# Kernel tuning notes

Measured on AMD Instinct MI355X. Metric: run time of the kernel, lower is better.

## Reference

```python
import jax, jax.numpy as jnp
import numpy as np
import math

H = 2048          # hidden_size
NH = 16           # num_attn_heads
HD = H // NH      # attn head dim = 128
NFW = 4           # num_lact_heads
FD = H // NFW     # fw head dim = 512
DH = FD           # inter_multi = 1.0
CHUNK = 512       # lact_chunk_size
WINDOW = 2048     # window_size
ROPE_BASE = 500000.0
BASE_LR_INV = math.log(math.expm1(0.001))  # inv_softplus(1e-3)


def rmsnorm(x, w, eps=1e-6):
    return x * jax.lax.rsqrt(jnp.mean(x * x, axis=-1, keepdims=True) + eps) * w


def l2norm(x, eps=1e-12):
    return x * jax.lax.rsqrt(jnp.sum(x * x, axis=-1, keepdims=True) + eps)


def rope(x):  # x: [b, h, s, d], half-split convention
    d = x.shape[-1]
    s = x.shape[2]
    inv = 1.0 / (ROPE_BASE ** (jnp.arange(d // 2, dtype=jnp.float32) / (d // 2)))
    f = jnp.arange(s, dtype=jnp.float32)[:, None] * inv[None, :]  # [s, d/2]
    cos, sin = jnp.cos(f), jnp.sin(f)
    x1, x2 = x[..., : d // 2], x[..., d // 2:]
    return jnp.concatenate([x1 * cos - x2 * sin, x2 * cos + x1 * sin], axis=-1)


def setup_inputs() -> dict:
    key = jax.random.key(0)
    ks = jax.random.split(key, 8)
    b, s = 2, 2048
    return {
        "hidden_states": jax.random.normal(ks[0], (b, s, H), jnp.float32),
        "qkv_w": jax.random.normal(ks[1], (3 * H, H), jnp.float32) / math.sqrt(H),
        "q_norm_w": jnp.ones((H,), jnp.float32),
        "k_norm_w": jnp.ones((H,), jnp.float32),
        "qk_scale": jnp.ones((H, 2), jnp.float32),
        "qk_offset": jnp.zeros((H, 2), jnp.float32),
        "lr_w": jax.random.normal(ks[2], (3 * NFW, H), jnp.float32) / math.sqrt(H),
        "lr_b": jnp.zeros((3 * NFW,), jnp.float32),
        "w0": jax.random.normal(ks[3], (NFW, DH, FD), jnp.float32) / math.sqrt(FD),
        "w1": jax.random.normal(ks[4], (NFW, FD, DH), jnp.float32) / math.sqrt(DH),
        "w2": jax.random.normal(ks[5], (NFW, DH, FD), jnp.float32) / math.sqrt(FD),
        "ttt_norm_w": jnp.ones((FD,), jnp.float32),
        "o_proj_w": jax.random.normal(ks[6], (H, H), jnp.float32) / math.sqrt(H),
    }


def reference(hidden_states, qkv_w, q_norm_w, k_norm_w, qk_scale, qk_offset,
              lr_w, lr_b, w0, w1, w2, ttt_norm_w, o_proj_w):
    x = hidden_states
    b, s, _ = x.shape
    nc = s // CHUNK

    qkv = x @ qkv_w.T
    q, k, v = jnp.split(qkv, 3, axis=-1)
    q = rmsnorm(q, q_norm_w)
    k = rmsnorm(k, k_norm_w)

    # ---- TTT (fast-weight SwiGLU) branch ----
    fq = jax.nn.silu(q * qk_scale[:, 0] + qk_offset[:, 0])
    fk = jax.nn.silu(k * qk_scale[:, 1] + qk_offset[:, 1])
    fv = jax.nn.silu(v)
    tohead = lambda t: t.reshape(b, s, NFW, FD).transpose(0, 2, 1, 3)  # [b,h,s,d]
    fq, fk, fv = l2norm(tohead(fq)), l2norm(tohead(fk)), tohead(fv)

    lr = jax.nn.softplus(x @ lr_w.T + lr_b + BASE_LR_INV)          # [b,s,3*NFW]
    lr = lr.reshape(b, s, 3, NFW).transpose(2, 0, 3, 1)[..., None]  # [3,b,h,s,1]
    lr0, lr1, lr2 = lr[0], lr[1], lr[2]

    chunkify = lambda t: t.reshape(b, NFW, nc, CHUNK, -1).transpose(2, 0, 1, 3, 4)
    qs, ks_, vs = chunkify(fq), chunkify(fk), chunkify(fv)
    l0s, l1s, l2s = chunkify(lr0), chunkify(lr1), chunkify(lr2)

    w0b = jnp.broadcast_to(w0, (b,) + w0.shape)
    w1b = jnp.broadcast_to(w1, (b,) + w1.shape)
    w2b = jnp.broadcast_to(w2, (b,) + w2.shape)

    def step(carry, xs):
        w0c, w1c, w2c = carry
        qc, kc, vc, l0, l1, l2 = xs
        # apply current fast weights to queries (strictly causal across chunks)
        hq = jax.nn.silu(jnp.einsum('bhcd,bhed->bhce', qc, w0c)) * \
             jnp.einsum('bhcd,bhed->bhce', qc, w2c)
        oc = jnp.einsum('bhce,bhde->bhcd', hq, w1c)
        # gradient-descent update on dot-product loss -sum(v * f(k))
        g1 = jnp.einsum('bhcd,bhed->bhce', kc, w0c)
        g2 = jnp.einsum('bhcd,bhed->bhce', kc, w2c)
        gate = jax.nn.silu(g1)
        hidden = gate * g2
        dhidden = jnp.einsum('bhcd,bhde->bhce', vc, w1c)  # w1^T v
        dh2 = dhidden * gate
        sig = jax.nn.sigmoid(g1)
        dh1 = dhidden * g2 * (sig * (1.0 + g1 * (1.0 - sig)))  # silu'(g1)
        w1n = w1c + jnp.einsum('bhcd,bhce->bhde', l1 * vc, hidden)
        w0n = w0c + jnp.einsum('bhce,bhcd->bhed', l0 * dh1, kc)
        w2n = w2c + jnp.einsum('bhce,bhcd->bhed', l2 * dh2, kc)
        return (w0n, w1n, w2n), oc

    _, o_chunks = jax.lax.scan(step, (w0b, w1b, w2b), (qs, ks_, vs, l0s, l1s, l2s))
    o_ttt = o_chunks.transpose(1, 2, 0, 3, 4).reshape(b, NFW, s, FD)
    o_ttt = rmsnorm(o_ttt, ttt_norm_w)
    o_ttt = o_ttt.transpose(0, 2, 1, 3).reshape(b, s, H)

    # ---- sliding-window attention branch ----
    qa = rope(q.reshape(b, s, NH, HD).transpose(0, 2, 1, 3))
    ka = rope(k.reshape(b, s, NH, HD).transpose(0, 2, 1, 3))
    va = v.reshape(b, s, NH, HD).transpose(0, 2, 1, 3)
    scores = jnp.einsum('bhqd,bhkd->bhqk', qa, ka) / math.sqrt(HD)
    i = jnp.arange(s)
    mask = (i[:, None] >= i[None, :]) & (i[:, None] - i[None, :] < WINDOW)
    scores = jnp.where(mask, scores, jnp.float32(-1e9))
    p = jax.nn.softmax(scores, axis=-1)
    attn = jnp.einsum('bhqk,bhkd->bhqd', p, va).transpose(0, 2, 1, 3).reshape(b, s, H)

    return (attn + o_ttt) @ o_proj_w.T
```

## Files before the change

kernel.cpp:

```cpp
#include <hip/hip_runtime.h>
#include <hip/hip_bf16.h>
#include <math.h>

using bf16 = __hip_bfloat16;

namespace {

constexpr int cH = 2048;
constexpr int cNH = 16;
constexpr int cHD = 128;
constexpr int cNFW = 4;
constexpr int cFD = 512;
constexpr int cS = 2048;
constexpr float cRSQRT_HD = 0.08838834764831845f;
constexpr long ZL_ = 262144;
constexpr long ZG_ = 1048576;

typedef __attribute__((ext_vector_type(8))) short short8;
typedef __attribute__((ext_vector_type(4))) float f32x4;

__device__ __forceinline__ float sigmoidf_(float x) { return 1.0f / (1.0f + __expf(-x)); }
__device__ __forceinline__ float b2f(bf16 v) { return __bfloat162float(v); }
__device__ __forceinline__ bf16 f2b(float v) { return __float2bfloat16(v); }
__device__ __forceinline__ unsigned short f2bu(float f) {
  return __builtin_bit_cast(unsigned short, __float2bfloat16(f));
}

#if defined(__has_builtin)
#if __has_builtin(__builtin_amdgcn_global_load_lds)
#define HAVE_GLOAD 1
#endif
#endif

__device__ __forceinline__ void gload16(const bf16* g, short* ldsbase) {
#ifdef HAVE_GLOAD
  __builtin_amdgcn_global_load_lds((const __attribute__((address_space(1))) void*)g,
                                   (__attribute__((address_space(3))) void*)ldsbase, 16, 0, 0);
#else
  const int l = threadIdx.x & 63;
  *(uint4*)(ldsbase + l * 8) = *(const uint4*)g;
#endif
}

__device__ __forceinline__ void stage16(const bf16* src, short* dst) {
  *(uint4*)dst = *(const uint4*)src;
  *(uint4*)(dst + 8) = *(const uint4*)(src + 8);
}

__device__ __forceinline__ void store1(float* p, float v) { *p = v; }
__device__ __forceinline__ void store1(bf16* p, float v) { *p = f2b(v); }

template <int AMODE, int BMODE>
__device__ __forceinline__ void mm_core(const bf16* __restrict__ Ab, int lda,
                                        const bf16* __restrict__ Bb, int ldb, int K,
                                        const float* __restrict__ sc,
                                        short* As, short* Bs, f32x4 acc[4][4]) {
  const int t = threadIdx.x, lane = t & 63, g = lane >> 4, c16 = lane & 15;
  const int wv = t >> 6, wm = (wv >> 1) * 64, wn = (wv & 1) * 64;
  for (int k0 = 0; k0 < K; k0 += 32) {
    __syncthreads();
    if constexpr (AMODE == 0) {
      const int ch = wv * 2;
      const bf16* g0 = Ab + (size_t)(ch * 16 + (lane >> 2)) * lda + k0 + (lane & 3) * 8;
      gload16(g0, &As[ch * 512]);
      gload16(g0 + (size_t)16 * lda, &As[ch * 512 + 512]);
    } else {
      const int kk = t >> 3, mseg = (t & 7) * 16;
      const float s = sc[k0 + kk];
      const bf16* p = Ab + (size_t)(k0 + kk) * lda + mseg;
#pragma unroll
      for (int i = 0; i < 16; ++i) As[(mseg + i) * 32 + kk] = (short)f2bu(b2f(p[i]) * s);
    }
    if constexpr (BMODE == 0) {
      const int ch = wv * 2;
      const bf16* g0 = Bb + (size_t)(ch * 16 + (lane >> 2)) * ldb + k0 + (lane & 3) * 8;
      gload16(g0, &Bs[ch * 512]);
      gload16(g0 + (size_t)16 * ldb, &Bs[ch * 512 + 512]);
    } else {
      const int kk = t >> 3, cseg = (t & 7) * 16;
      const short* p = (const short*)(Bb + (size_t)(k0 + kk) * ldb + cseg);
#pragma unroll
      for (int i = 0; i < 16; ++i) Bs[(cseg + i) * 32 + kk] = p[i];
    }
    __syncthreads();
    short8 af[4], bfr[4];
#pragma unroll
    for (int mi = 0; mi < 4; ++mi) af[mi] = *(const short8*)&As[(wm + mi * 16 + c16) * 32 + g * 8];
#pragma unroll
    for (int ni = 0; ni < 4; ++ni) bfr[ni] = *(const short8*)&Bs[(wn + ni * 16 + c16) * 32 + g * 8];
#pragma unroll
    for (int mi = 0; mi < 4; ++mi)
#pragma unroll
      for (int ni = 0; ni < 4; ++ni)
        acc[mi][ni] = __builtin_amdgcn_mfma_f32_16x16x32_bf16(af[mi], bfr[ni], acc[mi][ni], 0, 0, 0);
  }
}

template <bool ACC, bool MIR, typename TC>
__device__ __forceinline__ void mm_store(TC* Cb, bf16* Mb, int ldc, int rb, int cb, f32x4 acc[4][4]) {
  const int t = threadIdx.x, lane = t & 63, g = lane >> 4, c16 = lane & 15;
  const int wv = t >> 6, wm = (wv >> 1) * 64, wn = (wv & 1) * 64;
  const int rbase = rb + wm, cbase = cb + wn;
#pragma unroll
  for (int mi = 0; mi < 4; ++mi)
#pragma unroll
    for (int ni = 0; ni < 4; ++ni) {
      const int col = cbase + ni * 16 + c16;
#pragma unroll
      for (int r = 0; r < 4; ++r) {
        const int row = rbase + mi * 16 + g * 4 + r;
        TC* cp = Cb + (size_t)row * ldc + col;
        if constexpr (ACC) {
          float nv = *cp + acc[mi][ni][r];
          *cp = nv;
          if constexpr (MIR) Mb[(size_t)row * ldc + col] = f2b(nv);
        } else {
          store1(cp, acc[mi][ni][r]);
        }
      }
    }
}

template <typename TC, int BMODE>
__global__ __launch_bounds__(256) void k_mm(const bf16* __restrict__ A, int lda, long zsa,
                                            const bf16* __restrict__ B, int ldb, long zsb,
                                            TC* __restrict__ C, int ldc, long zsc, int K) {
  __shared__ short As[128 * 32];
  __shared__ short Bs[128 * 32];
  const int z = blockIdx.z;
  const bf16* Ab = A + (size_t)z * zsa + (size_t)blockIdx.y * 128 * lda;
  const bf16* Bb = (BMODE == 0) ? (B + (size_t)z * zsb + (size_t)blockIdx.x * 128 * ldb)
                                : (B + (size_t)z * zsb + blockIdx.x * 128);
  f32x4 acc[4][4];
  const f32x4 zero4 = {0.f, 0.f, 0.f, 0.f};
#pragma unroll
  for (int i = 0; i < 4; ++i)
#pragma unroll
    for (int j = 0; j < 4; ++j) acc[i][j] = zero4;
  mm_core<0, BMODE>(Ab, lda, Bb, ldb, K, nullptr, As, Bs, acc);
  mm_store<false, false>(C + (size_t)z * zsc, (bf16*)nullptr, ldc, blockIdx.y * 128, blockIdx.x * 128, acc);
}

__global__ __launch_bounds__(256) void k_fuse1(const bf16* __restrict__ fq, const bf16* __restrict__ fk,
                                               const bf16* __restrict__ fv,
                                               const bf16* __restrict__ w0b, const bf16* __restrict__ w1b,
                                               const bf16* __restrict__ w2b,
                                               bf16* __restrict__ hq, bf16* __restrict__ trH,
                                               bf16* __restrict__ trD1, bf16* __restrict__ trD2,
                                               const float* __restrict__ lr0, const float* __restrict__ lr2,
                                               int chunk) {
  __shared__ short S[12288];
  const int id = blockIdx.x, bh = id >> 6, tile = id & 63, by = tile >> 3, bx = tile & 7;
  const int t = threadIdx.x, lane = t & 63, g = lane >> 4, c16 = lane & 15, wv = t >> 6;
  const int wm = (wv >> 1) * 32, wn = (wv & 1) * 32;
  const size_t choff = (size_t)chunk * 262144;
  const bf16* Aq = fq + (size_t)bh * ZG_ + choff + (size_t)(by * 64) * cFD;
  const bf16* Ak = fk + (size_t)bh * ZG_ + choff + (size_t)(by * 64) * cFD;
  const bf16* Av = fv + (size_t)bh * ZG_ + choff + (size_t)(by * 64) * cFD;
  const bf16* B0 = w0b + (size_t)bh * ZL_ + (size_t)(bx * 64) * cFD;
  const bf16* B2 = w2b + (size_t)bh * ZL_ + (size_t)(bx * 64) * cFD;
  const bf16* B1 = w1b + (size_t)bh * ZL_ + bx * 64;

  f32x4 acc[5][2][2];
  const f32x4 zero4 = {0.f, 0.f, 0.f, 0.f};
#pragma unroll
  for (int v = 0; v < 5; ++v)
#pragma unroll
    for (int i = 0; i < 2; ++i)
#pragma unroll
      for (int j = 0; j < 2; ++j) acc[v][i][j] = zero4;

  const int srow = wv * 16 + (lane >> 2), scol = (lane & 3) * 8;
  for (int k0 = 0; k0 < 512; k0 += 32) {
    __syncthreads();
    gload16(Aq + (size_t)srow * cFD + k0 + scol, &S[0 + wv * 512]);
    gload16(Ak + (size_t)srow * cFD + k0 + scol, &S[2048 + wv * 512]);
    gload16(Av + (size_t)srow * cFD + k0 + scol, &S[4096 + wv * 512]);
    gload16(B0 + (size_t)srow * cFD + k0 + scol, &S[6144 + wv * 512]);
    gload16(B2 + (size_t)srow * cFD + k0 + scol, &S[8192 + wv * 512]);
    {
      const int kk = t >> 3, e8 = (t & 7) * 8;
      const short* p = (const short*)(B1 + (size_t)(k0 + kk) * cFD + e8);
#pragma unroll
      for (int i = 0; i < 8; ++i) S[10240 + (e8 + i) * 32 + kk] = p[i];
    }
    __syncthreads();
    short8 aq[2], ak[2], av[2], b0[2], b2[2], b1[2];
#pragma unroll
    for (int mi = 0; mi < 2; ++mi) {
      const int ro = (wm + mi * 16 + c16) * 32 + g * 8;
      aq[mi] = *(const short8*)&S[0 + ro];
      ak[mi] = *(const short8*)&S[2048 + ro];
      av[mi] = *(const short8*)&S[4096 + ro];
    }
#pragma unroll
    for (int ni = 0; ni < 2; ++ni) {
      const int ro = (wn + ni * 16 + c16) * 32 + g * 8;
      b0[ni] = *(const short8*)&S[6144 + ro];
      b2[ni] = *(const short8*)&S[8192 + ro];
      b1[ni] = *(const short8*)&S[10240 + ro];
    }
#pragma unroll
    for (int mi = 0; mi < 2; ++mi)
#pragma unroll
      for (int ni = 0; ni < 2; ++ni) {
        acc[0][mi][ni] = __builtin_amdgcn_mfma_f32_16x16x32_bf16(aq[mi], b0[ni], acc[0][mi][ni], 0, 0, 0);
        acc[1][mi][ni] = __builtin_amdgcn_mfma_f32_16x16x32_bf16(aq[mi], b2[ni], acc[1][mi][ni], 0, 0, 0);
        acc[2][mi][ni] = __builtin_amdgcn_mfma_f32_16x16x32_bf16(ak[mi], b0[ni], acc[2][mi][ni], 0, 0, 0);
        acc[3][mi][ni] = __builtin_amdgcn_mfma_f32_16x16x32_bf16(ak[mi], b2[ni], acc[3][mi][ni], 0, 0, 0);
        acc[4][mi][ni] = __builtin_amdgcn_mfma_f32_16x16x32_bf16(av[mi], b1[ni], acc[4][mi][ni], 0, 0, 0);
      }
  }

  float l0v[2][4], l2v[2][4];
#pragma unroll
  for (int mi = 0; mi < 2; ++mi)
#pragma unroll
    for (int r = 0; r < 4; ++r) {
      const int row = by * 64 + wm + mi * 16 + g * 4 + r;
      l0v[mi][r] = lr0[bh * 2048 + chunk * 512 + row];
      l2v[mi][r] = lr2[bh * 2048 + chunk * 512 + row];
    }
#pragma unroll
  for (int mi = 0; mi < 2; ++mi)
#pragma unroll
    for (int ni = 0; ni < 2; ++ni)
#pragma unroll
      for (int r = 0; r < 4; ++r) {
        float hq1 = acc[0][mi][ni][r], hq2 = acc[1][mi][ni][r];
        float g1 = acc[2][mi][ni][r], g2 = acc[3][mi][ni][r], dh = acc[4][mi][ni][r];
        acc[0][mi][ni][r] = hq1 * sigmoidf_(hq1) * hq2;
        float sg = sigmoidf_(g1);
        float gate = g1 * sg;
        acc[1][mi][ni][r] = gate * g2;
        acc[2][mi][ni][r] = l0v[mi][r] * dh * g2 * (sg * (1.0f + g1 * (1.0f - sg)));
        acc[3][mi][ni][r] = l2v[mi][r] * dh * gate;
      }

  short* Ts = S;
  bf16* dst0 = hq + (size_t)bh * ZL_;
  bf16* dstT[3] = {trH + (size_t)bh * ZL_, trD1 + (size_t)bh * ZL_, trD2 + (size_t)bh * ZL_};
#pragma unroll
  for (int rd = 0; rd < 4; ++rd) {
    __syncthreads();
#pragma unroll
    for (int mi = 0; mi < 2; ++mi)
#pragma unroll
      for (int ni = 0; ni < 2; ++ni)
#pragma unroll
        for (int r = 0; r < 4; ++r) {
          const int row = wm + mi * 16 + g * 4 + r, col = wn + ni * 16 + c16;
          if (rd == 0) Ts[row * 66 + col] = (short)f2bu(acc[0][mi][ni][r]);
          else Ts[col * 66 + row] = (short)f2bu(acc[rd][mi][ni][r]);
        }
    __syncthreads();
    const int rr = t >> 2, cs = (t & 3) * 16;
    unsigned short u[16] __attribute__((aligned(16)));
#pragma unroll
    for (int i = 0; i < 16; ++i) u[i] = (unsigned short)Ts[rr * 66 + cs + i];
    bf16* dp = (rd == 0) ? (dst0 + (size_t)(by * 64 + rr) * cFD + bx * 64 + cs)
                         : (dstT[rd - 1] + (size_t)(bx * 64 + rr) * cFD + by * 64 + cs);
    *(uint4*)dp = *(uint4*)u;
    *(uint4*)(dp + 8) = *(uint4*)(u + 8);
  }
}

__global__ __launch_bounds__(256) void k_octr(const bf16* __restrict__ hq, const bf16* __restrict__ w1b,
                                              bf16* __restrict__ occ,
                                              const bf16* __restrict__ fkb, const bf16* __restrict__ fvb,
                                              bf16* trK, bf16* trV, const float* __restrict__ lr1,
                                              int chunk) {
  __shared__ short Sh[8192];
  const int id = blockIdx.x, t = threadIdx.x;
  const size_t choff = (size_t)chunk * 262144;
  if (id < 128) {
    short* As = Sh;
    short* Bs = Sh + 4096;
    const int bh = id >> 4, by = (id >> 2) & 3, bx = id & 3;
    const bf16* Ab = hq + (size_t)bh * ZL_ + (size_t)by * 128 * cFD;
    const bf16* Bb = w1b + (size_t)bh * ZL_ + (size_t)bx * 128 * cFD;
    f32x4 acc[4][4];
    const f32x4 zero4 = {0.f, 0.f, 0.f, 0.f};
#pragma unroll
    for (int i = 0; i < 4; ++i)
#pragma unroll
      for (int j = 0; j < 4; ++j) acc[i][j] = zero4;
    mm_core<0, 0>(Ab, cFD, Bb, cFD, cFD, nullptr, As, Bs, acc);
    mm_store<false, false>(occ + (size_t)bh * ZL_, (bf16*)nullptr, cFD, by * 128, bx * 128, acc);
  } else {
    short* Ts = Sh;
    const int id2 = id - 128;
    const int var = id2 >> 9, bh = (id2 >> 6) & 7, by = (id2 >> 3) & 7, bx = id2 & 7;
    const bf16* src = ((var == 0) ? fkb : fvb) + choff + (size_t)bh * ZG_;
    bf16* dst = ((var == 0) ? trK : trV) + (size_t)bh * ZL_;
    {
      const int rr = t >> 2, cseg = (t & 3) * 16;
      if (var == 0) {
        const bf16* p = src + (size_t)(by * 64 + rr) * cFD + bx * 64 + cseg;
        stage16(p, &Ts[rr * 72 + cseg]);
      } else {
        const float s = lr1[bh * 2048 + chunk * 512 + by * 64 + rr];
        const bf16* p = src + (size_t)(by * 64 + rr) * cFD + bx * 64 + cseg;
        unsigned short u[16] __attribute__((aligned(16)));
#pragma unroll
        for (int i = 0; i < 16; ++i) u[i] = f2bu(b2f(p[i]) * s);
        *(uint4*)&Ts[rr * 72 + cseg] = *(uint4*)u;
        *(uint4*)&Ts[rr * 72 + cseg + 8] = *(uint4*)(u + 8);
      }
    }
    __syncthreads();
    {
      const int oc_ = t >> 2, rseg = (t & 3) * 16;
      unsigned short u[16] __attribute__((aligned(16)));
#pragma unroll
      for (int i = 0; i < 16; ++i) u[i] = (unsigned short)Ts[(rseg + i) * 72 + oc_];
      bf16* dp = dst + (size_t)(bx * 64 + oc_) * cFD + by * 64 + rseg;
      *(uint4*)dp = *(uint4*)u;
      *(uint4*)(dp + 8) = *(uint4*)(u + 8);
    }
  }
}

__global__ __launch_bounds__(256) void k_updna(const bf16* __restrict__ trV, const bf16* __restrict__ trH,
                                               const bf16* __restrict__ trD1, const bf16* __restrict__ trD2,
                                               const bf16* __restrict__ trK,
                                               float* w0s, float* w1s, float* w2s,
                                               bf16* w0b, bf16* w1b, bf16* w2b,
                                               const bf16* __restrict__ occ, const float* __restrict__ tw,
                                               bf16* __restrict__ y, int chunk) {
  __shared__ short Sh[8192];
  __shared__ float red[4];
  const int id = blockIdx.x, t = threadIdx.x;
  if (id < 384) {
    short* As = Sh;
    short* Bs = Sh + 4096;
    const int z = id >> 4, tile = id & 15, by = tile >> 2, bx = tile & 3;
    const int var = z >> 3, bh = z & 7;
    const bf16 *Aa, *Bb;
    float* W;
    bf16* M;
    if (var == 0) {
      Aa = trV + (size_t)bh * ZL_ + (size_t)by * 128 * cFD;
      Bb = trH + (size_t)bh * ZL_ + (size_t)bx * 128 * cFD;
      W = w1s + (size_t)bh * ZL_; M = w1b + (size_t)bh * ZL_;
    } else if (var == 1) {
      Aa = trD1 + (size_t)bh * ZL_ + (size_t)by * 128 * cFD;
      Bb = trK + (size_t)bh * ZL_ + (size_t)bx * 128 * cFD;
      W = w0s + (size_t)bh * ZL_; M = w0b + (size_t)bh * ZL_;
    } else {
      Aa = trD2 + (size_t)bh * ZL_ + (size_t)by * 128 * cFD;
      Bb = trK + (size_t)bh * ZL_ + (size_t)bx * 128 * cFD;
      W = w2s + (size_t)bh * ZL_; M = w2b + (size_t)bh * ZL_;
    }
    f32x4 acc[4][4];
    const f32x4 zero4 = {0.f, 0.f, 0.f, 0.f};
#pragma unroll
    for (int i = 0; i < 4; ++i)
#pragma unroll
      for (int j = 0; j < 4; ++j) acc[i][j] = zero4;
    mm_core<0, 0>(Aa, cFD, Bb, cFD, cFD, nullptr, As, Bs, acc);
    mm_store<true, true>(W, M, cFD, by * 128, bx * 128, acc);
  } else {
    const int rrow = id - 384;
    const int bh = rrow >> 9, rr = rrow & 511;
    const bf16* src = occ + ((size_t)bh * 512 + rr) * 512;
    float v0 = b2f(src[t]), v1 = b2f(src[t + 256]);
    float ss = v0 * v0 + v1 * v1;
    for (int d = 32; d; d >>= 1) ss += __shfl_down(ss, d);
    if ((t & 63) == 0) red[t >> 6] = ss;
    __syncthreads();
    const float rstd = rsqrtf((red[0] + red[1] + red[2] + red[3]) / cFD + 1e-6f);
    const int si = chunk * 512 + rr;
    bf16* dst = y + ((size_t)((bh >> 2) * cS) + si) * cH + (bh & 3) * cFD;
    dst[t] = f2b(b2f(dst[t]) + v0 * rstd * tw[t]);
    dst[t + 256] = f2b(b2f(dst[t + 256]) + v1 * rstd * tw[t + 256]);
  }
}

__global__ __launch_bounds__(256) void k_cvt(const float* __restrict__ src, bf16* __restrict__ dst) {
  const size_t i = ((size_t)blockIdx.x * 256 + threadIdx.x) * 8;
  float4 a = *(const float4*)(src + i), b = *(const float4*)(src + i + 4);
  unsigned short u[8] __attribute__((aligned(16)));
  u[0] = f2bu(a.x); u[1] = f2bu(a.y); u[2] = f2bu(a.z); u[3] = f2bu(a.w);
  u[4] = f2bu(b.x); u[5] = f2bu(b.y); u[6] = f2bu(b.z); u[7] = f2bu(b.w);
  *(uint4*)(dst + i) = *(uint4*)u;
}

__global__ __launch_bounds__(256) void k_winit(const float* __restrict__ w0, const float* __restrict__ w1,
                                               const float* __restrict__ w2,
                                               float* __restrict__ w0s, float* __restrict__ w1s,
                                               float* __restrict__ w2s) {
  const size_t i = (size_t)blockIdx.x * 256 + threadIdx.x;
  const int bh = (int)(i >> 18);
  const int f = bh & 3;
  const size_t off = i & 262143;
  const float* src; float* dst;
  if (blockIdx.y == 0) { src = w0; dst = w0s; }
  else if (blockIdx.y == 1) { src = w1; dst = w1s; }
  else { src = w2; dst = w2s; }
  dst[i] = src[(size_t)f * 262144 + off];
}

__global__ __launch_bounds__(64) void k_rope_tab(float* __restrict__ ct, float* __restrict__ stb) {
  const int si = blockIdx.x, j = threadIdx.x;
  float inv = powf(500000.0f, -(float)j / 64.0f);
  float ang = (float)si * inv;
  ct[(size_t)si * 64 + j] = cosf(ang);
  stb[(size_t)si * 64 + j] = sinf(ang);
}

__global__ __launch_bounds__(256) void k_lr(const float* __restrict__ x, const float* __restrict__ lr_w,
                                            const float* __restrict__ lr_b,
                                            float* lr0, float* lr1, float* lr2, float base) {
  const int token = blockIdx.x, b_ = token >> 11, si = token & 2047;
  const int wv = threadIdx.x >> 6, lane = threadIdx.x & 63;
  const float* xr = x + (size_t)token * cH;
#pragma unroll
  for (int jj = 0; jj < 3; ++jj) {
    const int j = wv * 3 + jj;
    const float* wr = lr_w + (size_t)j * cH;
    float s = 0.f;
    for (int k = lane; k < cH; k += 64) s += xr[k] * wr[k];
    for (int d = 32; d; d >>= 1) s += __shfl_down(s, d);
    if (lane == 0) {
      float v = s + lr_b[j] + base;
      float sp = (v > 15.f) ? v : log1pf(expf(v));
      const int tt = j >> 2, f = j & 3;
      float* dst = (tt == 0 ? lr0 : tt == 1 ? lr1 : lr2);
      dst[(size_t)(b_ * cNFW + f) * cS + si] = sp;
    }
  }
}

__global__ __launch_bounds__(256) void k_normrope(bf16* __restrict__ qkvh,
                                                  const float* __restrict__ qnw, const float* __restrict__ knw,
                                                  const float* __restrict__ ct, const float* __restrict__ stb,
                                                  bf16* __restrict__ qa, bf16* __restrict__ ka) {
  const int token = blockIdx.x, b_ = token >> 11, si = token & 2047;
  const int t = threadIdx.x;
  __shared__ float buf[cH];
  __shared__ float red[4];
  bf16* base = qkvh + (size_t)token * 3 * cH;
  for (int pass = 0; pass < 2; ++pass) {
    __syncthreads();
    bf16* src = base + pass * cH;
    const float* nw = pass ? knw : qnw;
    float ss = 0.f;
    for (int i = t; i < cH; i += 256) {
      float v = b2f(src[i]);
      buf[i] = v;
      ss += v * v;
    }
    for (int d = 32; d; d >>= 1) ss += __shfl_down(ss, d);
    if ((t & 63) == 0) red[t >> 6] = ss;
    __syncthreads();
    const float rstd = rsqrtf((red[0] + red[1] + red[2] + red[3]) / cH + 1e-6f);
    for (int i = t; i < cH; i += 256) {
      float v = buf[i] * rstd * nw[i];
      buf[i] = v;
      src[i] = f2b(v);
    }
    __syncthreads();
    bf16* dst = pass ? ka : qa;
    const float scale = pass ? 1.f : cRSQRT_HD;
    const int hh = t >> 4, j0 = (t & 15) * 4;
    const float* cr = ct + (size_t)si * 64 + j0;
    const float* sr = stb + (size_t)si * 64 + j0;
    bf16* drow = dst + ((size_t)(b_ * cNH + hh) * cS + si) * cHD;
    unsigned short u1[4] __attribute__((aligned(8))), u2[4] __attribute__((aligned(8)));
#pragma unroll
    for (int i = 0; i < 4; ++i) {
      float x1 = buf[hh * cHD + j0 + i], x2 = buf[hh * cHD + 64 + j0 + i];
      u1[i] = f2bu((x1 * cr[i] - x2 * sr[i]) * scale);
      u2[i] = f2bu((x2 * cr[i] + x1 * sr[i]) * scale);
    }
    *(uint2*)(drow + j0) = *(uint2*)u1;
    *(uint2*)(drow + 64 + j0) = *(uint2*)u2;
  }
}

__global__ __launch_bounds__(256) void k_vtr(const bf16* __restrict__ qkvh, bf16* __restrict__ vt) {
  const int tile = blockIdx.x, h = blockIdx.y, b_ = blockIdx.z;
  __shared__ short Ts[64 * 136];
  const int t = threadIdx.x;
  {
    const int r = t >> 2, seg = (t & 3) * 32;
    const bf16* src = qkvh + ((size_t)(b_ * cS) + tile * 64 + r) * 3 * cH + 2 * cH + h * cHD + seg;
    stage16(src, &Ts[r * 136 + seg]);
    stage16(src + 16, &Ts[r * 136 + seg + 16]);
  }
  __syncthreads();
  {
    const int d = t >> 1, seg2 = (t & 1) * 32;
    unsigned short u[32] __attribute__((aligned(16)));
#pragma unroll
    for (int i = 0; i < 32; ++i) u[i] = (unsigned short)Ts[(seg2 + i) * 136 + d];
    bf16* dp = vt + ((size_t)(b_ * cNH + h) * cHD + d) * cS + tile * 64 + seg2;
    *(uint4*)dp = *(uint4*)u;
    *(uint4*)(dp + 8) = *(uint4*)(u + 8);
    *(uint4*)(dp + 16) = *(uint4*)(u + 16);
    *(uint4*)(dp + 24) = *(uint4*)(u + 24);
  }
}

__global__ __launch_bounds__(256) void k_fqkv(const bf16* __restrict__ qkvh,
                                              const float* __restrict__ qk_scale,
                                              const float* __restrict__ qk_offset,
                                              bf16* fq, bf16* fk, bf16* fv) {
  const int token = blockIdx.x, b_ = token >> 11, si = token & 2047;
  const int t = threadIdx.x;
  const bf16* base = qkvh + (size_t)token * 3 * cH;
#pragma unroll
  for (int pass = 0; pass < 2; ++pass) {
    const bf16* src = base + pass * cH;
    bf16* fdst = pass ? fk : fq;
    const int head = t >> 6, lane = t & 63;
    float f[8];
    float ss2 = 0.f;
#pragma unroll
    for (int k = 0; k < 8; ++k) {
      const int idx = head * cFD + lane + k * 64;
      float v = b2f(src[idx]);
      float u = v * qk_scale[idx * 2 + pass] + qk_offset[idx * 2 + pass];
      float fv_ = u * sigmoidf_(u);
      f[k] = fv_;
      ss2 += fv_ * fv_;
    }
    for (int d = 1; d < 64; d <<= 1) ss2 += __shfl_xor(ss2, d);
    const float sc2 = rsqrtf(ss2 + 1e-12f);
    bf16* dst = fdst + ((size_t)(b_ * cNFW + head) * cS + si) * cFD;
#pragma unroll
    for (int k = 0; k < 8; ++k) dst[lane + k * 64] = f2b(f[k] * sc2);
  }
  const bf16* vr = base + 2 * cH;
  for (int i = t; i < cH; i += 256) {
    float v = b2f(vr[i]);
    fv[((size_t)(b_ * cNFW + (i >> 9)) * cS + si) * cFD + (i & 511)] = f2b(v * sigmoidf_(v));
  }
}

__global__ __launch_bounds__(256) void k_attn4(const bf16* __restrict__ qa, const bf16* __restrict__ ka,
                                               const bf16* __restrict__ vt, bf16* __restrict__ y) {
  const int id = blockIdx.x;
  const int hb = ((id >> 8) << 3) + (id & 7);
  const int qt = 31 - ((id >> 3) & 31);
  const int h = hb & 15, b_ = hb >> 4;
  const int q0 = qt * 64;
  __shared__ short Ks[64 * 136];
  __shared__ short Vts[128 * 72];
  const int t = threadIdx.x, lane = t & 63, g = lane >> 4, c16 = lane & 15, wv = t >> 6;
  const size_t hbq = (size_t)(b_ * cNH + h) * cS;
  const bf16* vb = vt + (size_t)(b_ * cNH + h) * (size_t)(cHD * cS);
  short8 qf[4];
  {
    const bf16* qsrc = qa + (hbq + q0 + wv * 16 + c16) * cHD;
#pragma unroll
    for (int ks = 0; ks < 4; ++ks) qf[ks] = *(const short8*)(qsrc + ks * 32 + g * 8);
  }
  f32x4 o[8];
  const f32x4 zero4 = {0.f, 0.f, 0.f, 0.f};
#pragma unroll
  for (int i = 0; i < 8; ++i) o[i] = zero4;
  float m[4], l[4];
#pragma unroll
  for (int r = 0; r < 4; ++r) { m[r] = -1e30f; l[r] = 0.f; }

  const int r = t >> 2, seg = (t & 3) * 32;
  const int dv = t >> 1, seg2 = (t & 1) * 32;
  uint4 kp0, kp1, kp2, kp3, vp0, vp1, vp2, vp3;
  {
    const bf16* ksrc = ka + (hbq + r) * cHD + seg;
    kp0 = *(const uint4*)ksrc; kp1 = *(const uint4*)(ksrc + 8);
    kp2 = *(const uint4*)(ksrc + 16); kp3 = *(const uint4*)(ksrc + 24);
    const bf16* vsrc = vb + (size_t)dv * cS + seg2;
    vp0 = *(const uint4*)vsrc; vp1 = *(const uint4*)(vsrc + 8);
    vp2 = *(const uint4*)(vsrc + 16); vp3 = *(const uint4*)(vsrc + 24);
  }

  for (int kt = 0; kt <= qt; ++kt) {
    __syncthreads();
    {
      short* kd = &Ks[r * 136 + seg];
      *(uint4*)kd = kp0; *(uint4*)(kd + 8) = kp1;
      *(uint4*)(kd + 16) = kp2; *(uint4*)(kd + 24) = kp3;
      short* vd = &Vts[dv * 72 + seg2];
      *(uint4*)vd = vp0; *(uint4*)(vd + 8) = vp1;
      *(uint4*)(vd + 16) = vp2; *(uint4*)(vd + 24) = vp3;
    }
    __syncthreads();
    if (kt < qt) {
      const bf16* ksrc = ka + (hbq + (kt + 1) * 64 + r) * cHD + seg;
      kp0 = *(const uint4*)ksrc; kp1 = *(const uint4*)(ksrc + 8);
      kp2 = *(const uint4*)(ksrc + 16); kp3 = *(const uint4*)(ksrc + 24);
      const bf16* vsrc = vb + (size_t)dv * cS + (kt + 1) * 64 + seg2;
      vp0 = *(const uint4*)vsrc; vp1 = *(const uint4*)(vsrc + 8);
      vp2 = *(const uint4*)(vsrc + 16); vp3 = *(const uint4*)(vsrc + 24);
    }

    f32x4 s4[4];
#pragma unroll
    for (int ni = 0; ni < 4; ++ni) s4[ni] = zero4;
    __builtin_amdgcn_s_setprio(1);
#pragma unroll
    for (int ks = 0; ks < 4; ++ks) {
#pragma unroll
      for (int ni = 0; ni < 4; ++ni) {
        short8 bb = *(const short8*)&Ks[(ni * 16 + c16) * 136 + ks * 32 + g * 8];
        s4[ni] = __builtin_amdgcn_mfma_f32_16x16x32_bf16(qf[ks], bb, s4[ni], 0, 0, 0);
      }
    }
    __builtin_amdgcn_s_setprio(0);
    __syncthreads();
    if (kt == qt) {
#pragma unroll
      for (int ni = 0; ni < 4; ++ni) {
        const int kv = kt * 64 + ni * 16 + c16;
#pragma unroll
        for (int rr = 0; rr < 4; ++rr) {
          const int qr = q0 + wv * 16 + g * 4 + rr;
          if (kv > qr) s4[ni][rr] = -1e9f;
        }
      }
    }
    float mx[4];
#pragma unroll
    for (int rr = 0; rr < 4; ++rr)
      mx[rr] = fmaxf(fmaxf(s4[0][rr], s4[1][rr]), fmaxf(s4[2][rr], s4[3][rr]));
#pragma unroll
    for (int d = 1; d < 16; d <<= 1)
#pragma unroll
      for (int rr = 0; rr < 4; ++rr) mx[rr] = fmaxf(mx[rr], __shfl_xor(mx[rr], d));
    bool need = false;
#pragma unroll
    for (int rr = 0; rr < 4; ++rr) need |= (mx[rr] > m[rr] + 8.f);
    if (__any(need)) {
      float corr[4];
#pragma unroll
      for (int rr = 0; rr < 4; ++rr) {
        float mn = fmaxf(m[rr], mx[rr]);
        corr[rr] = __expf(m[rr] - mn);
        m[rr] = mn;
      }
#pragma unroll
      for (int rr = 0; rr < 4; ++rr) l[rr] *= corr[rr];
#pragma unroll
      for (int nf = 0; nf < 8; ++nf)
#pragma unroll
        for (int rr = 0; rr < 4; ++rr) o[nf][rr] *= corr[rr];
    }
    float psum[4] = {0.f, 0.f, 0.f, 0.f};
#pragma unroll
    for (int ni = 0; ni < 4; ++ni)
#pragma unroll
      for (int rr = 0; rr < 4; ++rr) {
        float p = __expf(s4[ni][rr] - m[rr]);
        s4[ni][rr] = p;
        psum[rr] += p;
      }
#pragma unroll
    for (int d = 1; d < 16; d <<= 1)
#pragma unroll
      for (int rr = 0; rr < 4; ++rr) psum[rr] += __shfl_xor(psum[rr], d);
#pragma unroll
    for (int rr = 0; rr < 4; ++rr) l[rr] += psum[rr];
    short* pw = &Ks[wv * 1152];
#pragma unroll
    for (int ni = 0; ni < 4; ++ni)
#pragma unroll
      for (int rr = 0; rr < 4; ++rr)
        pw[(g * 4 + rr) * 72 + ni * 16 + c16] = (short)f2bu(s4[ni][rr]);
    __builtin_amdgcn_s_setprio(1);
#pragma unroll
    for (int ks2 = 0; ks2 < 2; ++ks2) {
      short8 a = *(const short8*)&pw[c16 * 72 + ks2 * 32 + g * 8];
#pragma unroll
      for (int nf = 0; nf < 8; ++nf) {
        short8 bb = *(const short8*)&Vts[(nf * 16 + c16) * 72 + ks2 * 32 + g * 8];
        o[nf] = __builtin_amdgcn_mfma_f32_16x16x32_bf16(a, bb, o[nf], 0, 0, 0);
      }
    }
    __builtin_amdgcn_s_setprio(0);
  }
  float inv[4];
#pragma unroll
  for (int rr = 0; rr < 4; ++rr) inv[rr] = 1.f / l[rr];
#pragma unroll
  for (int nf = 0; nf < 8; ++nf)
#pragma unroll
    for (int rr = 0; rr < 4; ++rr) {
      const size_t row = (size_t)(b_ * cS) + q0 + wv * 16 + g * 4 + rr;
      y[row * cH + h * cHD + nf * 16 + c16] = f2b(o[nf][rr] * inv[rr]);
    }
}

}

extern "C" void kernel_launch(void* const* d_in, const int* in_sizes, int n_in,
                              void* d_out, int out_size, void* d_ws, size_t ws_size,
                              hipStream_t stream) {
  (void)in_sizes; (void)n_in; (void)out_size; (void)ws_size;
  const float* x         = (const float*)d_in[0];
  const float* qkv_w     = (const float*)d_in[1];
  const float* q_norm_w  = (const float*)d_in[2];
  const float* k_norm_w  = (const float*)d_in[3];
  const float* qk_scale  = (const float*)d_in[4];
  const float* qk_offset = (const float*)d_in[5];
  const float* lr_w      = (const float*)d_in[6];
  const float* lr_b      = (const float*)d_in[7];
  const float* w0        = (const float*)d_in[8];
  const float* w1        = (const float*)d_in[9];
  const float* w2        = (const float*)d_in[10];
  const float* ttt_nw    = (const float*)d_in[11];
  const float* o_proj_w  = (const float*)d_in[12];
  float* out = (float*)d_out;

  char* Wb = (char*)d_ws;
  bf16* qkvh = (bf16*)Wb;
  bf16* hq   = (bf16*)(Wb + 0UL);
  bf16* trH  = (bf16*)(Wb + 4194304UL);
  bf16* trD1 = (bf16*)(Wb + 8388608UL);
  bf16* trD2 = (bf16*)(Wb + 12582912UL);
  bf16* trK  = (bf16*)(Wb + 16777216UL);
  bf16* trV  = (bf16*)(Wb + 20971520UL);
  bf16* occ  = (bf16*)(Wb + 29360128UL);
  bf16* w0b  = (bf16*)(Wb + 33554432UL);
  bf16* w1b  = (bf16*)(Wb + 37748736UL);
  bf16* w2b  = (bf16*)(Wb + 41943040UL);
  bf16* opwb = (bf16*)(Wb + 0UL);
  size_t off = 50331648UL;
  bf16* fqb = (bf16*)(Wb + off); off += 16777216UL;
  bf16* fkb = (bf16*)(Wb + off); off += 16777216UL;
  bf16* fvb = (bf16*)(Wb + off); off += 16777216UL;
  float* w0s = (float*)(Wb + off); off += 8388608UL;
  float* w1s = (float*)(Wb + off); off += 8388608UL;
  float* w2s = (float*)(Wb + off); off += 8388608UL;
  float* lr0 = (float*)(Wb + off); off += 65536UL;
  float* lr1 = (float*)(Wb + off); off += 65536UL;
  float* lr2 = (float*)(Wb + off); off += 65536UL;
  bf16* y = (bf16*)(Wb + off); off += 16777216UL;
  float* ct  = (float*)(Wb + off); off += 524288UL;
  float* stb = (float*)(Wb + off); off += 524288UL;
  bf16* xb = fqb;
  bf16* qkvwb = fkb;
  bf16* qa = fqb;
  bf16* ka = fkb;
  bf16* vt = fvb;

  const float base_lr_inv = logf(expm1f(0.001f));
  dim3 blk(256);

  k_winit<<<dim3(8192, 3), blk, 0, stream>>>(w0, w1, w2, w0s, w1s, w2s);
  k_rope_tab<<<dim3(2048), dim3(64), 0, stream>>>(ct, stb);
  k_cvt<<<dim3(4096), blk, 0, stream>>>(x, xb);
  k_cvt<<<dim3(6144), blk, 0, stream>>>(qkv_w, qkvwb);
  k_mm<bf16, 0><<<dim3(48, 32, 1), blk, 0, stream>>>(xb, 2048, 0, qkvwb, 2048, 0, qkvh, 6144, 0, 2048);
  k_lr<<<dim3(4096), blk, 0, stream>>>(x, lr_w, lr_b, lr0, lr1, lr2, base_lr_inv);
  k_normrope<<<dim3(4096), blk, 0, stream>>>(qkvh, q_norm_w, k_norm_w, ct, stb, qa, ka);
  k_vtr<<<dim3(32, 16, 2), blk, 0, stream>>>(qkvh, vt);
  k_attn4<<<dim3(1024), blk, 0, stream>>>(qa, ka, vt, y);
  k_fqkv<<<dim3(4096), blk, 0, stream>>>(qkvh, qk_scale, qk_offset, fqb, fkb, fvb);
  k_cvt<<<dim3(3072), blk, 0, stream>>>(w0s, w0b);

  for (int c = 0; c < 4; ++c) {
    k_fuse1<<<dim3(512), blk, 0, stream>>>(fqb, fkb, fvb, w0b, w1b, w2b,
                                           hq, trH, trD1, trD2, lr0, lr2, c);
    k_octr<<<dim3(1152), blk, 0, stream>>>(hq, w1b, occ, fkb, fvb, trK, trV, lr1, c);
    k_updna<<<dim3(4480), blk, 0, stream>>>(trV, trH, trD1, trD2, trK,
                                            w0s, w1s, w2s, w0b, w1b, w2b, occ, ttt_nw, y, c);
  }
  k_cvt<<<dim3(2048), blk, 0, stream>>>(o_proj_w, opwb);
  k_mm<float, 0><<<dim3(16, 32, 1), blk, 0, stream>>>(y, 2048, 0, opwb, 2048, 0, out, 2048, 0, 2048);
}
```

Baseline: 806.8 us.

## Merge per-chunk TTT kernels into two launches with double-buffered w1 and occ

Removes the k_octr kernel per chunk. The hq·w1 output GEMM moves into k_updna, where it runs alongside the weight-update GEMMs. The K/V transposes move into k_fuse1. To let the output GEMM read the old w1 while the update writes the new one, w1 bf16 and the occ buffer are double-buffered. The previous chunk's rmsnorm-and-accumulate into y is deferred into the next k_fuse1, with a final k_norm launch for the last chunk. The attention kernel is also replaced by a new k_attn5 variant using half as many blocks. This cuts launches and serialization per chunk at the cost of more buffers and larger mixed-role grids.

```diff
diff --git a/kernel.cpp b/kernel.cpp
--- a/kernel.cpp
+++ b/kernel.cpp
@@ -143,161 +143,144 @@
 
 __global__ __launch_bounds__(256) void k_fuse1(const bf16* __restrict__ fq, const bf16* __restrict__ fk,
                                                const bf16* __restrict__ fv,
-                                               const bf16* __restrict__ w0b, const bf16* __restrict__ w1b,
+                                               const bf16* __restrict__ w0b, const bf16* __restrict__ w1bc,
                                                const bf16* __restrict__ w2b,
                                                bf16* __restrict__ hq, bf16* __restrict__ trH,
                                                bf16* __restrict__ trD1, bf16* __restrict__ trD2,
-                                               const float* __restrict__ lr0, const float* __restrict__ lr2,
+                                               bf16* __restrict__ trK, bf16* __restrict__ trV,
+                                               const float* __restrict__ lr0, const float* __restrict__ lr1,
+                                               const float* __restrict__ lr2,
+                                               const bf16* __restrict__ occPrev,
+                                               const float* __restrict__ tw, bf16* __restrict__ y,
                                                int chunk) {
   __shared__ short S[12288];
-  const int id = blockIdx.x, bh = id >> 6, tile = id & 63, by = tile >> 3, bx = tile & 7;
-  const int t = threadIdx.x, lane = t & 63, g = lane >> 4, c16 = lane & 15, wv = t >> 6;
-  const int wm = (wv >> 1) * 32, wn = (wv & 1) * 32;
-  const size_t choff = (size_t)chunk * 262144;
-  const bf16* Aq = fq + (size_t)bh * ZG_ + choff + (size_t)(by * 64) * cFD;
-  const bf16* Ak = fk + (size_t)bh * ZG_ + choff + (size_t)(by * 64) * cFD;
-  const bf16* Av = fv + (size_t)bh * ZG_ + choff + (size_t)(by * 64) * cFD;
-  const bf16* B0 = w0b + (size_t)bh * ZL_ + (size_t)(bx * 64) * cFD;
-  const bf16* B2 = w2b + (size_t)bh * ZL_ + (size_t)(bx * 64) * cFD;
-  const bf16* B1 = w1b + (size_t)bh * ZL_ + bx * 64;
-
-  f32x4 acc[5][2][2];
-  const f32x4 zero4 = {0.f, 0.f, 0.f, 0.f};
-#pragma unroll
-  for (int v = 0; v < 5; ++v)
-#pragma unroll
-    for (int i = 0; i < 2; ++i)
-#pragma unroll
-      for (int j = 0; j < 2; ++j) acc[v][i][j] = zero4;
-
-  const int srow = wv * 16 + (lane >> 2), scol = (lane & 3) * 8;
-  for (int k0 = 0; k0 < 512; k0 += 32) {
-    __syncthreads();
-    gload16(Aq + (size_t)srow * cFD + k0 + scol, &S[0 + wv * 512]);
-    gload16(Ak + (size_t)srow * cFD + k0 + scol, &S[2048 + wv * 512]);
-    gload16(Av + (size_t)srow * cFD + k0 + scol, &S[4096 + wv * 512]);
-    gload16(B0 + (size_t)srow * cFD + k0 + scol, &S[6144 + wv * 512]);
-    gload16(B2 + (size_t)srow * cFD + k0 + scol, &S[8192 + wv * 512]);
-    {
-      const int kk = t >> 3, e8 = (t & 7) * 8;
-      const short* p = (const short*)(B1 + (size_t)(k0 + kk) * cFD + e8);
-#pragma unroll
-      for (int i = 0; i < 8; ++i) S[10240 + (e8 + i) * 32 + kk] = p[i];
-    }
-    __syncthreads();
-    short8 aq[2], ak[2], av[2], b0[2], b2[2], b1[2];
-#pragma unroll
-    for (int mi = 0; mi < 2; ++mi) {
-      const int ro = (wm + mi * 16 + c16) * 32 + g * 8;
-      aq[mi] = *(const short8*)&S[0 + ro];
-      ak[mi] = *(const short8*)&S[2048 + ro];
-      av[mi] = *(const short8*)&S[4096 + ro];
-    }
-#pragma unroll
-    for (int ni = 0; ni < 2; ++ni) {
-      const int ro = (wn + ni * 16 + c16) * 32 + g * 8;
-      b0[ni] = *(const short8*)&S[6144 + ro];
-      b2[ni] = *(const short8*)&S[8192 + ro];
-      b1[ni] = *(const short8*)&S[10240 + ro];
-    }
-#pragma unroll
-    for (int mi = 0; mi < 2; ++mi)
-#pragma unroll
-      for (int ni = 0; ni < 2; ++ni) {
-        acc[0][mi][ni] = __builtin_amdgcn_mfma_f32_16x16x32_bf16(aq[mi], b0[ni], acc[0][mi][ni], 0, 0, 0);
-        acc[1][mi][ni] = __builtin_amdgcn_mfma_f32_16x16x32_bf16(aq[mi], b2[ni], acc[1][mi][ni], 0, 0, 0);
-        acc[2][mi][ni] = __builtin_amdgcn_mfma_f32_16x16x32_bf16(ak[mi], b0[ni], acc[2][mi][ni], 0, 0, 0);
-        acc[3][mi][ni] = __builtin_amdgcn_mfma_f32_16x16x32_bf16(ak[mi], b2[ni], acc[3][mi][ni], 0, 0, 0);
-        acc[4][mi][ni] = __builtin_amdgcn_mfma_f32_16x16x32_bf16(av[mi], b1[ni], acc[4][mi][ni], 0, 0, 0);
-      }
-  }
-
-  float l0v[2][4], l2v[2][4];
-#pragma unroll
-  for (int mi = 0; mi < 2; ++mi)
-#pragma unroll
-    for (int r = 0; r < 4; ++r) {
-      const int row = by * 64 + wm + mi * 16 + g * 4 + r;
-      l0v[mi][r] = lr0[bh * 2048 + chunk * 512 + row];
-      l2v[mi][r] = lr2[bh * 2048 + chunk * 512 + row];
-    }
-#pragma unroll
-  for (int mi = 0; mi < 2; ++mi)
-#pragma unroll
-    for (int ni = 0; ni < 2; ++ni)
-#pragma unroll
-      for (int r = 0; r < 4; ++r) {
-        float hq1 = acc[0][mi][ni][r], hq2 = acc[1][mi][ni][r];
-        float g1 = acc[2][mi][ni][r], g2 = acc[3][mi][ni][r], dh = acc[4][mi][ni][r];
-        acc[0][mi][ni][r] = hq1 * sigmoidf_(hq1) * hq2;
-        float sg = sigmoidf_(g1);
-        float gate = g1 * sg;
-        acc[1][mi][ni][r] = gate * g2;
-        acc[2][mi][ni][r] = l0v[mi][r] * dh * g2 * (sg * (1.0f + g1 * (1.0f - sg)));
-        acc[3][mi][ni][r] = l2v[mi][r] * dh * gate;
-      }
-
-  short* Ts = S;
-  bf16* dst0 = hq + (size_t)bh * ZL_;
-  bf16* dstT[3] = {trH + (size_t)bh * ZL_, trD1 + (size_t)bh * ZL_, trD2 + (size_t)bh * ZL_};
-#pragma unroll
-  for (int rd = 0; rd < 4; ++rd) {
-    __syncthreads();
-#pragma unroll
-    for (int mi = 0; mi < 2; ++mi)
-#pragma unroll
-      for (int ni = 0; ni < 2; ++ni)
-#pragma unroll
-        for (int r = 0; r < 4; ++r) {
-          const int row = wm + mi * 16 + g * 4 + r, col = wn + ni * 16 + c16;
-          if (rd == 0) Ts[row * 66 + col] = (short)f2bu(acc[0][mi][ni][r]);
-          else Ts[col * 66 + row] = (short)f2bu(acc[rd][mi][ni][r]);
-        }
-    __syncthreads();
-    const int rr = t >> 2, cs = (t & 3) * 16;
-    unsigned short u[16] __attribute__((aligned(16)));
-#pragma unroll
-    for (int i = 0; i < 16; ++i) u[i] = (unsigned short)Ts[rr * 66 + cs + i];
-    bf16* dp = (rd == 0) ? (dst0 + (size_t)(by * 64 + rr) * cFD + bx * 64 + cs)
-                         : (dstT[rd - 1] + (size_t)(bx * 64 + rr) * cFD + by * 64 + cs);
-    *(uint4*)dp = *(uint4*)u;
-    *(uint4*)(dp + 8) = *(uint4*)(u + 8);
-  }
-}
-
-__global__ __launch_bounds__(256) void k_octr(const bf16* __restrict__ hq, const bf16* __restrict__ w1b,
-                                              bf16* __restrict__ occ,
-                                              const bf16* __restrict__ fkb, const bf16* __restrict__ fvb,
-                                              bf16* trK, bf16* trV, const float* __restrict__ lr1,
-                                              int chunk) {
-  __shared__ short Sh[8192];
+  __shared__ float red[4];
   const int id = blockIdx.x, t = threadIdx.x;
   const size_t choff = (size_t)chunk * 262144;
-  if (id < 128) {
-    short* As = Sh;
-    short* Bs = Sh + 4096;
-    const int bh = id >> 4, by = (id >> 2) & 3, bx = id & 3;
-    const bf16* Ab = hq + (size_t)bh * ZL_ + (size_t)by * 128 * cFD;
-    const bf16* Bb = w1b + (size_t)bh * ZL_ + (size_t)bx * 128 * cFD;
-    f32x4 acc[4][4];
+
+  if (id < 512) {
+    const int bh = id >> 6, tile = id & 63, by = tile >> 3, bx = tile & 7;
+    const int lane = t & 63, g = lane >> 4, c16 = lane & 15, wv = t >> 6;
+    const int wm = (wv >> 1) * 32, wn = (wv & 1) * 32;
+    const bf16* Aq = fq + (size_t)bh * ZG_ + choff + (size_t)(by * 64) * cFD;
+    const bf16* Ak = fk + (size_t)bh * ZG_ + choff + (size_t)(by * 64) * cFD;
+    const bf16* Av = fv + (size_t)bh * ZG_ + choff + (size_t)(by * 64) * cFD;
+    const bf16* B0 = w0b + (size_t)bh * ZL_ + (size_t)(bx * 64) * cFD;
+    const bf16* B2 = w2b + (size_t)bh * ZL_ + (size_t)(bx * 64) * cFD;
+    const bf16* B1 = w1bc + (size_t)bh * ZL_ + bx * 64;
+
+    f32x4 acc[5][2][2];
     const f32x4 zero4 = {0.f, 0.f, 0.f, 0.f};
 #pragma unroll
-    for (int i = 0; i < 4; ++i)
-#pragma unroll
-      for (int j = 0; j < 4; ++j) acc[i][j] = zero4;
-    mm_core<0, 0>(Ab, cFD, Bb, cFD, cFD, nullptr, As, Bs, acc);
-    mm_store<false, false>(occ + (size_t)bh * ZL_, (bf16*)nullptr, cFD, by * 128, bx * 128, acc);
-  } else {
-    short* Ts = Sh;
-    const int id2 = id - 128;
+    for (int v = 0; v < 5; ++v)
+#pragma unroll
+      for (int i = 0; i < 2; ++i)
+#pragma unroll
+        for (int j = 0; j < 2; ++j) acc[v][i][j] = zero4;
+
+    const int srow = wv * 16 + (lane >> 2), scol = (lane & 3) * 8;
+    for (int k0 = 0; k0 < 512; k0 += 32) {
+      __syncthreads();
+      gload16(Aq + (size_t)srow * cFD + k0 + scol, &S[0 + wv * 512]);
+      gload16(Ak + (size_t)srow * cFD + k0 + scol, &S[2048 + wv * 512]);
+      gload16(Av + (size_t)srow * cFD + k0 + scol, &S[4096 + wv * 512]);
+      gload16(B0 + (size_t)srow * cFD + k0 + scol, &S[6144 + wv * 512]);
+      gload16(B2 + (size_t)srow * cFD + k0 + scol, &S[8192 + wv * 512]);
+      {
+        const int kk = t >> 3, e8 = (t & 7) * 8;
+        const short* p = (const short*)(B1 + (size_t)(k0 + kk) * cFD + e8);
+#pragma unroll
+        for (int i = 0; i < 8; ++i) S[10240 + (e8 + i) * 32 + kk] = p[i];
+      }
+      __syncthreads();
+      short8 aq[2], ak[2], av[2], b0[2], b2[2], b1[2];
+#pragma unroll
+      for (int mi = 0; mi < 2; ++mi) {
+        const int ro = (wm + mi * 16 + c16) * 32 + g * 8;
+        aq[mi] = *(const short8*)&S[0 + ro];
+        ak[mi] = *(const short8*)&S[2048 + ro];
+        av[mi] = *(const short8*)&S[4096 + ro];
+      }
+#pragma unroll
+      for (int ni = 0; ni < 2; ++ni) {
+        const int ro = (wn + ni * 16 + c16) * 32 + g * 8;
+        b0[ni] = *(const short8*)&S[6144 + ro];
+        b2[ni] = *(const short8*)&S[8192 + ro];
+        b1[ni] = *(const short8*)&S[10240 + ro];
+      }
+#pragma unroll
+      for (int mi = 0; mi < 2; ++mi)
+#pragma unroll
+        for (int ni = 0; ni < 2; ++ni) {
+          acc[0][mi][ni] = __builtin_amdgcn_mfma_f32_16x16x32_bf16(aq[mi], b0[ni], acc[0][mi][ni], 0, 0, 0);
+          acc[1][mi][ni] = __builtin_amdgcn_mfma_f32_16x16x32_bf16(aq[mi], b2[ni], acc[1][mi][ni], 0, 0, 0);
+          acc[2][mi][ni] = __builtin_amdgcn_mfma_f32_16x16x32_bf16(ak[mi], b0[ni], acc[2][mi][ni], 0, 0, 0);
+          acc[3][mi][ni] = __builtin_amdgcn_mfma_f32_16x16x32_bf16(ak[mi], b2[ni], acc[3][mi][ni], 0, 0, 0);
+          acc[4][mi][ni] = __builtin_amdgcn_mfma_f32_16x16x32_bf16(av[mi], b1[ni], acc[4][mi][ni], 0, 0, 0);
+        }
+    }
+
+    float l0v[2][4], l2v[2][4];
+#pragma unroll
+    for (int mi = 0; mi < 2; ++mi)
+#pragma unroll
+      for (int r = 0; r < 4; ++r) {
+        const int row = by * 64 + wm + mi * 16 + g * 4 + r;
+        l0v[mi][r] = lr0[bh * 2048 + chunk * 512 + row];
+        l2v[mi][r] = lr2[bh * 2048 + chunk * 512 + row];
+      }
+#pragma unroll
+    for (int mi = 0; mi < 2; ++mi)
+#pragma unroll
+      for (int ni = 0; ni < 2; ++ni)
+#pragma unroll
+        for (int r = 0; r < 4; ++r) {
+          float hq1 = acc[0][mi][ni][r], hq2 = acc[1][mi][ni][r];
+          float g1 = acc[2][mi][ni][r], g2 = acc[3][mi][ni][r], dh = acc[4][mi][ni][r];
+          acc[0][mi][ni][r] = hq1 * sigmoidf_(hq1) * hq2;
+          float sg = sigmoidf_(g1);
+          float gate = g1 * sg;
+          acc[1][mi][ni][r] = gate * g2;
+          acc[2][mi][ni][r] = l0v[mi][r] * dh * g2 * (sg * (1.0f + g1 * (1.0f - sg)));
+          acc[3][mi][ni][r] = l2v[mi][r] * dh * gate;
+        }
+
+    short* Ts = S;
+    bf16* dst0 = hq + (size_t)bh * ZL_;
+    bf16* dstT[3] = {trH + (size_t)bh * ZL_, trD1 + (size_t)bh * ZL_, trD2 + (size_t)bh * ZL_};
+#pragma unroll
+    for (int rd = 0; rd < 4; ++rd) {
+      __syncthreads();
+#pragma unroll
+      for (int mi = 0; mi < 2; ++mi)
+#pragma unroll
+        for (int ni = 0; ni < 2; ++ni)
+#pragma unroll
+          for (int r = 0; r < 4; ++r) {
+            const int row = wm + mi * 16 + g * 4 + r, col = wn + ni * 16 + c16;
+            if (rd == 0) Ts[row * 66 + col] = (short)f2bu(acc[0][mi][ni][r]);
+            else Ts[col * 66 + row] = (short)f2bu(acc[rd][mi][ni][r]);
+          }
+      __syncthreads();
+      const int rr = t >> 2, cs = (t & 3) * 16;
+      unsigned short u[16] __attribute__((aligned(16)));
+#pragma unroll
+      for (int i = 0; i < 16; ++i) u[i] = (unsigned short)Ts[rr * 66 + cs + i];
+      bf16* dp = (rd == 0) ? (dst0 + (size_t)(by * 64 + rr) * cFD + bx * 64 + cs)
+                           : (dstT[rd - 1] + (size_t)(bx * 64 + rr) * cFD + by * 64 + cs);
+      *(uint4*)dp = *(uint4*)u;
+      *(uint4*)(dp + 8) = *(uint4*)(u + 8);
+    }
+  } else if (id < 1536) {
+    short* Ts = S;
+    const int id2 = id - 512;
     const int var = id2 >> 9, bh = (id2 >> 6) & 7, by = (id2 >> 3) & 7, bx = id2 & 7;
-    const bf16* src = ((var == 0) ? fkb : fvb) + choff + (size_t)bh * ZG_;
+    const bf16* src = ((var == 0) ? fk : fv) + choff + (size_t)bh * ZG_;
     bf16* dst = ((var == 0) ? trK : trV) + (size_t)bh * ZL_;
     {
       const int rr = t >> 2, cseg = (t & 3) * 16;
       if (var == 0) {
-        const bf16* p = src + (size_t)(by * 64 + rr) * cFD + bx * 64 + cseg;
-        stage16(p, &Ts[rr * 72 + cseg]);
+        stage16(src + (size_t)(by * 64 + rr) * cFD + bx * 64 + cseg, &Ts[rr * 72 + cseg]);
       } else {
         const float s = lr1[bh * 2048 + chunk * 512 + by * 64 + rr];
         const bf16* p = src + (size_t)(by * 64 + rr) * cFD + bx * 64 + cseg;
@@ -318,18 +301,31 @@
       *(uint4*)dp = *(uint4*)u;
       *(uint4*)(dp + 8) = *(uint4*)(u + 8);
     }
+  } else {
+    const int rrow = id - 1536;
+    const int bh = rrow >> 9, rr = rrow & 511;
+    const bf16* src = occPrev + ((size_t)bh * 512 + rr) * 512;
+    float v0 = b2f(src[t]), v1 = b2f(src[t + 256]);
+    float ss = v0 * v0 + v1 * v1;
+    for (int d = 32; d; d >>= 1) ss += __shfl_down(ss, d);
+    if ((t & 63) == 0) red[t >> 6] = ss;
+    __syncthreads();
+    const float rstd = rsqrtf((red[0] + red[1] + red[2] + red[3]) / cFD + 1e-6f);
+    const int si = (chunk - 1) * 512 + rr;
+    bf16* dst = y + ((size_t)((bh >> 2) * cS) + si) * cH + (bh & 3) * cFD;
+    dst[t] = f2b(b2f(dst[t]) + v0 * rstd * tw[t]);
+    dst[t + 256] = f2b(b2f(dst[t + 256]) + v1 * rstd * tw[t + 256]);
   }
 }
 
 __global__ __launch_bounds__(256) void k_updna(const bf16* __restrict__ trV, const bf16* __restrict__ trH,
                                                const bf16* __restrict__ trD1, const bf16* __restrict__ trD2,
                                                const bf16* __restrict__ trK,
+                                               const bf16* __restrict__ hq, const bf16* __restrict__ w1bc,
                                                float* w0s, float* w1s, float* w2s,
-                                               bf16* w0b, bf16* w1b, bf16* w2b,
-                                               const bf16* __restrict__ occ, const float* __restrict__ tw,
-                                               bf16* __restrict__ y, int chunk) {
+                                               bf16* w0b, bf16* w1bn, bf16* w2b,
+                                               bf16* __restrict__ occCur) {
   __shared__ short Sh[8192];
-  __shared__ float red[4];
   const int id = blockIdx.x, t = threadIdx.x;
   if (id < 384) {
     short* As = Sh;
@@ -342,7 +338,7 @@
     if (var == 0) {
       Aa = trV + (size_t)bh * ZL_ + (size_t)by * 128 * cFD;
       Bb = trH + (size_t)bh * ZL_ + (size_t)bx * 128 * cFD;
-      W = w1s + (size_t)bh * ZL_; M = w1b + (size_t)bh * ZL_;
+      W = w1s + (size_t)bh * ZL_; M = w1bn + (size_t)bh * ZL_;
     } else if (var == 1) {
       Aa = trD1 + (size_t)bh * ZL_ + (size_t)by * 128 * cFD;
       Bb = trK + (size_t)bh * ZL_ + (size_t)bx * 128 * cFD;
@@ -361,20 +357,72 @@
     mm_core<0, 0>(Aa, cFD, Bb, cFD, cFD, nullptr, As, Bs, acc);
     mm_store<true, true>(W, M, cFD, by * 128, bx * 128, acc);
   } else {
-    const int rrow = id - 384;
-    const int bh = rrow >> 9, rr = rrow & 511;
-    const bf16* src = occ + ((size_t)bh * 512 + rr) * 512;
-    float v0 = b2f(src[t]), v1 = b2f(src[t + 256]);
-    float ss = v0 * v0 + v1 * v1;
-    for (int d = 32; d; d >>= 1) ss += __shfl_down(ss, d);
-    if ((t & 63) == 0) red[t >> 6] = ss;
-    __syncthreads();
-    const float rstd = rsqrtf((red[0] + red[1] + red[2] + red[3]) / cFD + 1e-6f);
-    const int si = chunk * 512 + rr;
-    bf16* dst = y + ((size_t)((bh >> 2) * cS) + si) * cH + (bh & 3) * cFD;
-    dst[t] = f2b(b2f(dst[t]) + v0 * rstd * tw[t]);
-    dst[t + 256] = f2b(b2f(dst[t + 256]) + v1 * rstd * tw[t + 256]);
-  }
+    const int id2 = id - 384;
+    const int bh = id2 >> 6, tile = id2 & 63, by = tile >> 3, bx = tile & 7;
+    const int lane = t & 63, g = lane >> 4, c16 = lane & 15, wv = t >> 6;
+    const int wm = (wv >> 1) * 32, wn = (wv & 1) * 32;
+    const bf16* Aa = hq + (size_t)bh * ZL_ + (size_t)(by * 64) * cFD;
+    const bf16* Bb = w1bc + (size_t)bh * ZL_ + (size_t)(bx * 64) * cFD;
+    short* As = Sh;
+    short* Bs = Sh + 2048;
+    f32x4 acc[2][2];
+    const f32x4 zero4 = {0.f, 0.f, 0.f, 0.f};
+#pragma unroll
+    for (int i = 0; i < 2; ++i)
+#pragma unroll
+      for (int j = 0; j < 2; ++j) acc[i][j] = zero4;
+    for (int k0 = 0; k0 < 512; k0 += 32) {
+      __syncthreads();
+      {
+        const int srow = wv * 16 + (lane >> 2), scol = (lane & 3) * 8;
+        gload16(Aa + (size_t)srow * cFD + k0 + scol, &As[wv * 512]);
+        gload16(Bb + (size_t)srow * cFD + k0 + scol, &Bs[wv * 512]);
+      }
+      __syncthreads();
+      short8 af[2], bfr[2];
+#pragma unroll
+      for (int mi = 0; mi < 2; ++mi) af[mi] = *(const short8*)&As[(wm + mi * 16 + c16) * 32 + g * 8];
+#pragma unroll
+      for (int ni = 0; ni < 2; ++ni) bfr[ni] = *(const short8*)&Bs[(wn + ni * 16 + c16) * 32 + g * 8];
+#pragma unroll
+      for (int mi = 0; mi < 2; ++mi)
+#pragma unroll
+        for (int ni = 0; ni < 2; ++ni)
+          acc[mi][ni] = __builtin_amdgcn_mfma_f32_16x16x32_bf16(af[mi], bfr[ni], acc[mi][ni], 0, 0, 0);
+    }
+    bf16* C = occCur + (size_t)bh * ZL_;
+#pragma unroll
+    for (int mi = 0; mi < 2; ++mi)
+#pragma unroll
+      for (int ni = 0; ni < 2; ++ni) {
+        const int col = bx * 64 + wn + ni * 16 + c16;
+#pragma unroll
+        for (int r = 0; r < 4; ++r) {
+          const int row = by * 64 + wm + mi * 16 + g * 4 + r;
+          C[(size_t)row * cFD + col] = f2b(acc[mi][ni][r]);
+        }
+      }
+  }
+}
+
+__global__ __launch_bounds__(256) void k_norm(const bf16* __restrict__ occ,
+                                              const float* __restrict__ tw, bf16* __restrict__ y,
+                                              int chunk) {
+  __shared__ float red[4];
+  const int rrow = blockIdx.x;
+  const int bh = rrow >> 9, rr = rrow & 511;
+  const int t = threadIdx.x;
+  const bf16* src = occ + ((size_t)bh * 512 + rr) * 512;
+  float v0 = b2f(src[t]), v1 = b2f(src[t + 256]);
+  float ss = v0 * v0 + v1 * v1;
+  for (int d = 32; d; d >>= 1) ss += __shfl_down(ss, d);
+  if ((t & 63) == 0) red[t >> 6] = ss;
+  __syncthreads();
+  const float rstd = rsqrtf((red[0] + red[1] + red[2] + red[3]) / cFD + 1e-6f);
+  const int si = chunk * 512 + rr;
+  bf16* dst = y + ((size_t)((bh >> 2) * cS) + si) * cH + (bh & 3) * cFD;
+  dst[t] = f2b(b2f(dst[t]) + v0 * rstd * tw[t]);
+  dst[t + 256] = f2b(b2f(dst[t + 256]) + v1 * rstd * tw[t + 256]);
 }
 
 __global__ __launch_bounds__(256) void k_cvt(const float* __restrict__ src, bf16* __restrict__ dst) {
@@ -539,158 +587,171 @@
   }
 }
 
-__global__ __launch_bounds__(256) void k_attn4(const bf16* __restrict__ qa, const bf16* __restrict__ ka,
+__global__ __launch_bounds__(256) void k_attn5(const bf16* __restrict__ qa, const bf16* __restrict__ ka,
                                                const bf16* __restrict__ vt, bf16* __restrict__ y) {
   const int id = blockIdx.x;
-  const int hb = ((id >> 8) << 3) + (id & 7);
-  const int qt = 31 - ((id >> 3) & 31);
+  const int xcd = id & 7;
+  const int j = id >> 3;
+  const int p = j & 15;
+  const int hb = (j >> 4) * 8 + xcd;
   const int h = hb & 15, b_ = hb >> 4;
-  const int q0 = qt * 64;
   __shared__ short Ks[64 * 136];
   __shared__ short Vts[128 * 72];
   const int t = threadIdx.x, lane = t & 63, g = lane >> 4, c16 = lane & 15, wv = t >> 6;
   const size_t hbq = (size_t)(b_ * cNH + h) * cS;
   const bf16* vb = vt + (size_t)(b_ * cNH + h) * (size_t)(cHD * cS);
-  short8 qf[4];
-  {
-    const bf16* qsrc = qa + (hbq + q0 + wv * 16 + c16) * cHD;
-#pragma unroll
-    for (int ks = 0; ks < 4; ++ks) qf[ks] = *(const short8*)(qsrc + ks * 32 + g * 8);
-  }
-  f32x4 o[8];
-  const f32x4 zero4 = {0.f, 0.f, 0.f, 0.f};
-#pragma unroll
-  for (int i = 0; i < 8; ++i) o[i] = zero4;
-  float m[4], l[4];
-#pragma unroll
-  for (int r = 0; r < 4; ++r) { m[r] = -1e30f; l[r] = 0.f; }
-
   const int r = t >> 2, seg = (t & 3) * 32;
   const int dv = t >> 1, seg2 = (t & 1) * 32;
-  uint4 kp0, kp1, kp2, kp3, vp0, vp1, vp2, vp3;
-  {
-    const bf16* ksrc = ka + (hbq + r) * cHD + seg;
-    kp0 = *(const uint4*)ksrc; kp1 = *(const uint4*)(ksrc + 8);
-    kp2 = *(const uint4*)(ksrc + 16); kp3 = *(const uint4*)(ksrc + 24);
-    const bf16* vsrc = vb + (size_t)dv * cS + seg2;
-    vp0 = *(const uint4*)vsrc; vp1 = *(const uint4*)(vsrc + 8);
-    vp2 = *(const uint4*)(vsrc + 16); vp3 = *(const uint4*)(vsrc + 24);
-  }
-
-  for (int kt = 0; kt <= qt; ++kt) {
-    __syncthreads();
+  const f32x4 zero4 = {0.f, 0.f, 0.f, 0.f};
+
+  for (int half = 0; half < 2; ++half) {
+    const int qt = half ? p : 31 - p;
+    const int q0 = qt * 64;
+    short8 qf[4];
     {
-      short* kd = &Ks[r * 136 + seg];
-      *(uint4*)kd = kp0; *(uint4*)(kd + 8) = kp1;
-      *(uint4*)(kd + 16) = kp2; *(uint4*)(kd + 24) = kp3;
-      short* vd = &Vts[dv * 72 + seg2];
-      *(uint4*)vd = vp0; *(uint4*)(vd + 8) = vp1;
-      *(uint4*)(vd + 16) = vp2; *(uint4*)(vd + 24) = vp3;
-    }
-    __syncthreads();
-    if (kt < qt) {
-      const bf16* ksrc = ka + (hbq + (kt + 1) * 64 + r) * cHD + seg;
+      const bf16* qsrc = qa + (hbq + q0 + wv * 16 + c16) * cHD;
+#pragma unroll
+      for (int ks = 0; ks < 4; ++ks) qf[ks] = *(const short8*)(qsrc + ks * 32 + g * 8);
+    }
+    f32x4 o[8];
+#pragma unroll
+    for (int i = 0; i < 8; ++i) o[i] = zero4;
+    float m[4], l[4];
+#pragma unroll
+    for (int rr = 0; rr < 4; ++rr) { m[rr] = -1e30f; l[rr] = 0.f; }
+
+    uint4 kp0, kp1, kp2, kp3, vp0, vp1, vp2, vp3;
+    {
+      const bf16* ksrc = ka + (hbq + r) * cHD + seg;
       kp0 = *(const uint4*)ksrc; kp1 = *(const uint4*)(ksrc + 8);
       kp2 = *(const uint4*)(ksrc + 16); kp3 = *(const uint4*)(ksrc + 24);
-      const bf16* vsrc = vb + (size_t)dv * cS + (kt + 1) * 64 + seg2;
+      const bf16* vsrc = vb + (size_t)dv * cS + seg2;
       vp0 = *(const uint4*)vsrc; vp1 = *(const uint4*)(vsrc + 8);
       vp2 = *(const uint4*)(vsrc + 16); vp3 = *(const uint4*)(vsrc + 24);
     }
 
-    f32x4 s4[4];
-#pragma unroll
-    for (int ni = 0; ni < 4; ++ni) s4[ni] = zero4;
-    __builtin_amdgcn_s_setprio(1);
-#pragma unroll
-    for (int ks = 0; ks < 4; ++ks) {
-#pragma unroll
-      for (int ni = 0; ni < 4; ++ni) {
-        short8 bb = *(const short8*)&Ks[(ni * 16 + c16) * 136 + ks * 32 + g * 8];
-        s4[ni] = __builtin_amdgcn_mfma_f32_16x16x32_bf16(qf[ks], bb, s4[ni], 0, 0, 0);
-      }
-    }
-    __builtin_amdgcn_s_setprio(0);
-    __syncthreads();
-    if (kt == qt) {
-#pragma unroll
-      for (int ni = 0; ni < 4; ++ni) {
-        const int kv = kt * 64 + ni * 16 + c16;
+    for (int kt = 0; kt <= qt; ++kt) {
+      __syncthreads();
+      {
+        short* kd = &Ks[r * 136 + seg];
+        *(uint4*)kd = kp0; *(uint4*)(kd + 8) = kp1;
+        *(uint4*)(kd + 16) = kp2; *(uint4*)(kd + 24) = kp3;
+        short* vd = &Vts[dv * 72 + seg2];
+        *(uint4*)vd = vp0; *(uint4*)(vd + 8) = vp1;
+        *(uint4*)(vd + 16) = vp2; *(uint4*)(vd + 24) = vp3;
+      }
+      __syncthreads();
+      if (kt < qt) {
+        const bf16* ksrc = ka + (hbq + (kt + 1) * 64 + r) * cHD + seg;
+        kp0 = *(const uint4*)ksrc; kp1 = *(const uint4*)(ksrc + 8);
+        kp2 = *(const uint4*)(ksrc + 16); kp3 = *(const uint4*)(ksrc + 24);
+        const bf16* vsrc = vb + (size_t)dv * cS + (kt + 1) * 64 + seg2;
+        vp0 = *(const uint4*)vsrc; vp1 = *(const uint4*)(vsrc + 8);
+        vp2 = *(const uint4*)(vsrc + 16); vp3 = *(const uint4*)(vsrc + 24);
+      } else if (half == 0) {
+        const bf16* ksrc = ka + (hbq + r) * cHD + seg;
+        kp0 = *(const uint4*)ksrc; kp1 = *(const uint4*)(ksrc + 8);
+        kp2 = *(const uint4*)(ksrc + 16); kp3 = *(const uint4*)(ksrc + 24);
+        const bf16* vsrc = vb + (size_t)dv * cS + seg2;
+        vp0 = *(const uint4*)vsrc; vp1 = *(const uint4*)(vsrc + 8);
+        vp2 = *(const uint4*)(vsrc + 16); vp3 = *(const uint4*)(vsrc + 24);
+      }
+
+      f32x4 s4[4];
+#pragma unroll
+      for (int ni = 0; ni < 4; ++ni) s4[ni] = zero4;
+      __builtin_amdgcn_s_setprio(1);
+#pragma unroll
+      for (int ks = 0; ks < 4; ++ks) {
+#pragma unroll
+        for (int ni = 0; ni < 4; ++ni) {
+          short8 bb = *(const short8*)&Ks[(ni * 16 + c16) * 136 + ks * 32 + g * 8];
+          s4[ni] = __builtin_amdgcn_mfma_f32_16x16x32_bf16(qf[ks], bb, s4[ni], 0, 0, 0);
+        }
+      }
+      __builtin_amdgcn_s_setprio(0);
+      __syncthreads();
+      if (kt == qt) {
+#pragma unroll
+        for (int ni = 0; ni < 4; ++ni) {
+          const int kv = kt * 64 + ni * 16 + c16;
+#pragma unroll
+          for (int rr = 0; rr < 4; ++rr) {
+            const int qr = q0 + wv * 16 + g * 4 + rr;
+            if (kv > qr) s4[ni][rr] = -1e9f;
+          }
+        }
+      }
+      float mx[4];
+#pragma unroll
+      for (int rr = 0; rr < 4; ++rr)
+        mx[rr] = fmaxf(fmaxf(s4[0][rr], s4[1][rr]), fmaxf(s4[2][rr], s4[3][rr]));
+#pragma unroll
+      for (int d = 1; d < 16; d <<= 1)
+#pragma unroll
+        for (int rr = 0; rr < 4; ++rr) mx[rr] = fmaxf(mx[rr], __shfl_xor(mx[rr], d));
+      bool need = false;
+#pragma unroll
+      for (int rr = 0; rr < 4; ++rr) need |= (mx[rr] > m[rr] + 8.f);
+      if (__any(need)) {
+        float corr[4];
 #pragma unroll
         for (int rr = 0; rr < 4; ++rr) {
-          const int qr = q0 + wv * 16 + g * 4 + rr;
-          if (kv > qr) s4[ni][rr] = -1e9f;
+          float mn = fmaxf(m[rr], mx[rr]);
+          corr[rr] = __expf(m[rr] - mn);
+          m[rr] = mn;
         }
-      }
-    }
-    float mx[4];
-#pragma unroll
-    for (int rr = 0; rr < 4; ++rr)
-      mx[rr] = fmaxf(fmaxf(s4[0][rr], s4[1][rr]), fmaxf(s4[2][rr], s4[3][rr]));
-#pragma unroll
-    for (int d = 1; d < 16; d <<= 1)
-#pragma unroll
-      for (int rr = 0; rr < 4; ++rr) mx[rr] = fmaxf(mx[rr], __shfl_xor(mx[rr], d));
-    bool need = false;
-#pragma unroll
-    for (int rr = 0; rr < 4; ++rr) need |= (mx[rr] > m[rr] + 8.f);
-    if (__any(need)) {
-      float corr[4];
+#pragma unroll
+        for (int rr = 0; rr < 4; ++rr) l[rr] *= corr[rr];
+#pragma unroll
+        for (int nf = 0; nf < 8; ++nf)
+#pragma unroll
+          for (int rr = 0; rr < 4; ++rr) o[nf][rr] *= corr[rr];
+      }
+      float psum[4] = {0.f, 0.f, 0.f, 0.f};
+#pragma unroll
+      for (int ni = 0; ni < 4; ++ni)
+#pragma unroll
+        for (int rr = 0; rr < 4; ++rr) {
+          float pp = __expf(s4[ni][rr] - m[rr]);
+          s4[ni][rr] = pp;
+          psum[rr] += pp;
+        }
+#pragma unroll
+      for (int d = 1; d < 16; d <<= 1)
+#pragma unroll
+        for (int rr = 0; rr < 4; ++rr) psum[rr] += __shfl_xor(psum[rr], d);
+#pragma unroll
+      for (int rr = 0; rr < 4; ++rr) l[rr] += psum[rr];
+      short* pw = &Ks[wv * 1152];
+#pragma unroll
+      for (int ni = 0; ni < 4; ++ni)
+#pragma unroll
+        for (int rr = 0; rr < 4; ++rr)
+          pw[(g * 4 + rr) * 72 + ni * 16 + c16] = (short)f2bu(s4[ni][rr]);
+      __builtin_amdgcn_s_setprio(1);
+#pragma unroll
+      for (int ks2 = 0; ks2 < 2; ++ks2) {
+        short8 a = *(const short8*)&pw[c16 * 72 + ks2 * 32 + g * 8];
+#pragma unroll
+        for (int nf = 0; nf < 8; ++nf) {
+          short8 bb = *(const short8*)&Vts[(nf * 16 + c16) * 72 + ks2 * 32 + g * 8];
+          o[nf] = __builtin_amdgcn_mfma_f32_16x16x32_bf16(a, bb, o[nf], 0, 0, 0);
+        }
+      }
+      __builtin_amdgcn_s_setprio(0);
+    }
+    float inv[4];
+#pragma unroll
+    for (int rr = 0; rr < 4; ++rr) inv[rr] = 1.f / l[rr];
+#pragma unroll
+    for (int nf = 0; nf < 8; ++nf)
 #pragma unroll
       for (int rr = 0; rr < 4; ++rr) {
-        float mn = fmaxf(m[rr], mx[rr]);
-        corr[rr] = __expf(m[rr] - mn);
-        m[rr] = mn;
-      }
-#pragma unroll
-      for (int rr = 0; rr < 4; ++rr) l[rr] *= corr[rr];
-#pragma unroll
-      for (int nf = 0; nf < 8; ++nf)
-#pragma unroll
-        for (int rr = 0; rr < 4; ++rr) o[nf][rr] *= corr[rr];
-    }
-    float psum[4] = {0.f, 0.f, 0.f, 0.f};
-#pragma unroll
-    for (int ni = 0; ni < 4; ++ni)
-#pragma unroll
-      for (int rr = 0; rr < 4; ++rr) {
-        float p = __expf(s4[ni][rr] - m[rr]);
-        s4[ni][rr] = p;
-        psum[rr] += p;
-      }
-#pragma unroll
-    for (int d = 1; d < 16; d <<= 1)
-#pragma unroll
-      for (int rr = 0; rr < 4; ++rr) psum[rr] += __shfl_xor(psum[rr], d);
-#pragma unroll
-    for (int rr = 0; rr < 4; ++rr) l[rr] += psum[rr];
-    short* pw = &Ks[wv * 1152];
-#pragma unroll
-    for (int ni = 0; ni < 4; ++ni)
-#pragma unroll
-      for (int rr = 0; rr < 4; ++rr)
-        pw[(g * 4 + rr) * 72 + ni * 16 + c16] = (short)f2bu(s4[ni][rr]);
-    __builtin_amdgcn_s_setprio(1);
-#pragma unroll
-    for (int ks2 = 0; ks2 < 2; ++ks2) {
-      short8 a = *(const short8*)&pw[c16 * 72 + ks2 * 32 + g * 8];
-#pragma unroll
-      for (int nf = 0; nf < 8; ++nf) {
-        short8 bb = *(const short8*)&Vts[(nf * 16 + c16) * 72 + ks2 * 32 + g * 8];
-        o[nf] = __builtin_amdgcn_mfma_f32_16x16x32_bf16(a, bb, o[nf], 0, 0, 0);
-      }
-    }
-    __builtin_amdgcn_s_setprio(0);
-  }
-  float inv[4];
-#pragma unroll
-  for (int rr = 0; rr < 4; ++rr) inv[rr] = 1.f / l[rr];
-#pragma unroll
-  for (int nf = 0; nf < 8; ++nf)
-#pragma unroll
-    for (int rr = 0; rr < 4; ++rr) {
-      const size_t row = (size_t)(b_ * cS) + q0 + wv * 16 + g * 4 + rr;
-      y[row * cH + h * cHD + nf * 16 + c16] = f2b(o[nf][rr] * inv[rr]);
-    }
+        const size_t row = (size_t)(b_ * cS) + q0 + wv * 16 + g * 4 + rr;
+        y[row * cH + h * cHD + nf * 16 + c16] = f2b(o[nf][rr] * inv[rr]);
+      }
+  }
 }
 
 }
@@ -722,10 +783,12 @@
   bf16* trD2 = (bf16*)(Wb + 12582912UL);
   bf16* trK  = (bf16*)(Wb + 16777216UL);
   bf16* trV  = (bf16*)(Wb + 20971520UL);
-  bf16* occ  = (bf16*)(Wb + 29360128UL);
+  bf16* occA = (bf16*)(Wb + 25165824UL);
+  bf16* occB = (bf16*)(Wb + 29360128UL);
   bf16* w0b  = (bf16*)(Wb + 33554432UL);
-  bf16* w1b  = (bf16*)(Wb + 37748736UL);
+  bf16* w1b0 = (bf16*)(Wb + 37748736UL);
   bf16* w2b  = (bf16*)(Wb + 41943040UL);
+  bf16* w1b1 = (bf16*)(Wb + 46137344UL);
   bf16* opwb = (bf16*)(Wb + 0UL);
   size_t off = 50331648UL;
   bf16* fqb = (bf16*)(Wb + off); off += 16777216UL;
@@ -745,6 +808,8 @@
   bf16* qa = fqb;
   bf16* ka = fkb;
   bf16* vt = fvb;
+  bf16* w1m[2] = {w1b0, w1b1};
+  bf16* occb[2] = {occA, occB};
 
   const float base_lr_inv = logf(expm1f(0.001f));
   dim3 blk(256);
@@ -757,17 +822,22 @@
   k_lr<<<dim3(4096), blk, 0, stream>>>(x, lr_w, lr_b, lr0, lr1, lr2, base_lr_inv);
   k_normrope<<<dim3(4096), blk, 0, stream>>>(qkvh, q_norm_w, k_norm_w, ct, stb, qa, ka);
   k_vtr<<<dim3(32, 16, 2), blk, 0, stream>>>(qkvh, vt);
-  k_attn4<<<dim3(1024), blk, 0, stream>>>(qa, ka, vt, y);
+  k_attn5<<<dim3(512), blk, 0, stream>>>(qa, ka, vt, y);
   k_fqkv<<<dim3(4096), blk, 0, stream>>>(qkvh, qk_scale, qk_offset, fqb, fkb, fvb);
   k_cvt<<<dim3(3072), blk, 0, stream>>>(w0s, w0b);
 
   for (int c = 0; c < 4; ++c) {
-    k_fuse1<<<dim3(512), blk, 0, stream>>>(fqb, fkb, fvb, w0b, w1b, w2b,
-                                           hq, trH, trD1, trD2, lr0, lr2, c);
-    k_octr<<<dim3(1152), blk, 0, stream>>>(hq, w1b, occ, fkb, fvb, trK, trV, lr1, c);
-    k_updna<<<dim3(4480), blk, 0, stream>>>(trV, trH, trD1, trD2, trK,
-                                            w0s, w1s, w2s, w0b, w1b, w2b, occ, ttt_nw, y, c);
-  }
+    const int g1 = (c == 0) ? 1536 : 5632;
+    k_fuse1<<<dim3(g1), blk, 0, stream>>>(fqb, fkb, fvb, w0b, w1m[c & 1], w2b,
+                                          hq, trH, trD1, trD2, trK, trV,
+                                          lr0, lr1, lr2,
+                                          (c == 0) ? occb[0] : occb[(c - 1) & 1],
+                                          ttt_nw, y, c);
+    k_updna<<<dim3(896), blk, 0, stream>>>(trV, trH, trD1, trD2, trK, hq, w1m[c & 1],
+                                           w0s, w1s, w2s, w0b, w1m[(c + 1) & 1], w2b,
+                                           occb[c & 1]);
+  }
+  k_norm<<<dim3(4096), blk, 0, stream>>>(occb[1], ttt_nw, y, 3);
   k_cvt<<<dim3(2048), blk, 0, stream>>>(o_proj_w, opwb);
   k_mm<float, 0><<<dim3(16, 32, 1), blk, 0, stream>>>(y, 2048, 0, opwb, 2048, 0, out, 2048, 0, 2048);
 }
```

After: 743.5 us. 1.09x faster.
